# Performance work log

Measured on AMD Instinct MI355X. Metric: run time of the kernel, lower is better.

## Reference

```python
import jax, jax.numpy as jnp
import numpy as np

T, B, IN, H, A = 512, 256, 292, 128, 12


def setup_inputs() -> dict:
    key = jax.random.key(0)
    ks = jax.random.split(key, 8)
    s = 1.0 / np.sqrt(H)
    return {
        "x": jax.random.normal(ks[0], (T, B, IN), dtype=jnp.float32),
        "done": jax.random.randint(ks[1], (T, B), 0, 2, dtype=jnp.int32),
        "h0": jax.random.normal(ks[2], (1, B, H), dtype=jnp.float32),
        "c0": jax.random.normal(ks[3], (1, B, H), dtype=jnp.float32),
        "W_ih": jax.random.normal(ks[4], (4 * H, IN), dtype=jnp.float32) * s,
        "W_hh": jax.random.normal(ks[5], (4 * H, H), dtype=jnp.float32) * s,
        "b_ih": jnp.zeros((4 * H,), dtype=jnp.float32),
        "b_hh": jnp.zeros((4 * H,), dtype=jnp.float32),
        "W_pi": jax.random.normal(ks[6], (A, H), dtype=jnp.float32) * 0.01,
        "b_pi": jnp.zeros((A,), dtype=jnp.float32),
        "W_v": jax.random.normal(ks[7], (1, H), dtype=jnp.float32),
        "b_v": jnp.zeros((1,), dtype=jnp.float32),
    }


def reference(x, done, h0, c0, W_ih, W_hh, b_ih, b_hh, W_pi, b_pi, W_v, b_v):
    # get_states: per-timestep LSTM with done-based reset of (h, c), as a scan.
    done_f = done.astype(x.dtype)  # [T, B]
    bias = b_ih + b_hh  # [4H]

    def step(carry, inp):
        h, c = carry  # [B, H] each
        x_t, d_t = inp  # [B, IN], [B]
        m = (1.0 - d_t)[:, None]  # reset mask
        h = h * m
        c = c * m
        # PyTorch LSTM gate order: input, forget, cell(g), output
        gates = x_t @ W_ih.T + h @ W_hh.T + bias  # [B, 4H]
        i, f, g, o = jnp.split(gates, 4, axis=-1)
        c = jax.nn.sigmoid(f) * c + jax.nn.sigmoid(i) * jnp.tanh(g)
        h = jax.nn.sigmoid(o) * jnp.tanh(c)
        return (h, c), h

    (hN, cN), hs = jax.lax.scan(step, (h0[0], c0[0]), (x, done_f))
    hidden = hs.reshape(T * B, H)  # flatten(cat(new_hidden), 0, 1)
    logits = hidden @ W_pi.T + b_pi  # policy_layers
    value = hidden @ W_v.T + b_v  # value_layers
    return jnp.concatenate([logits, value], axis=-1)  # [T*B, A+1]
```

## Files before the change

kernel.cpp:

```cpp
#include <hip/hip_runtime.h>
#include <stdint.h>
#include <stddef.h>

#define T_ 512
#define B_ 256
#define IN_ 292
#define H_ 128
#define G4_ 512
#define TB_ 131072
#define LCH 32
#define NCH 16
#define KP_ 320

typedef short bf16x8 __attribute__((ext_vector_type(8)));
typedef float f32x4 __attribute__((ext_vector_type(4)));

__device__ __forceinline__ unsigned short f2bf(float f) {
  unsigned u = __float_as_uint(f);
  u += 0x7FFFu + ((u >> 16) & 1u);
  return (unsigned short)(u >> 16);
}
__device__ __forceinline__ float bf2f(unsigned short s) {
  return __uint_as_float(((unsigned)s) << 16);
}
__device__ __forceinline__ unsigned bfpack2(float a, float b) {
  unsigned ua = __float_as_uint(a) + 0x8000u;
  unsigned ub = __float_as_uint(b) + 0x8000u;
  return __builtin_amdgcn_perm(ub, ua, 0x07060302u);
}
__device__ __forceinline__ float sigf(float x) {
  return __builtin_amdgcn_rcpf(1.0f + __expf(-x));
}
__device__ __forceinline__ float tanhf_(float x) {
  return 1.0f - 2.0f * __builtin_amdgcn_rcpf(__expf(2.0f * x) + 1.0f);
}
__device__ __forceinline__ void barrier_lds() {
  asm volatile("s_waitcnt lgkmcnt(0)\n\ts_barrier" ::: "memory");
}
__device__ __forceinline__ void load_pr(const unsigned short* p, ushort4* pr) {
  union { uint4 v; ushort4 s[2]; } a, b;
  a.v = *(const uint4*)p;
  b.v = *(const uint4*)(p + 8);
  pr[0] = a.s[0]; pr[1] = a.s[1]; pr[2] = b.s[0]; pr[3] = b.s[1];
}

__global__ __launch_bounds__(256) void k0w_cvt(
    const float* __restrict__ Wih, const float* __restrict__ bih,
    const float* __restrict__ bhh, unsigned short* __restrict__ Wb,
    float* __restrict__ bias2) {
  const int g = blockIdx.x * 256 + threadIdx.x;
  const int jj = g / 40, s = g % 40;
  const int src = (jj & 3) * 128 + (jj >> 2);
  if (g < 512) {
    const int sb = (g & 3) * 128 + (g >> 2);
    bias2[g] = bih[sb] + bhh[sb];
  }
  float4 a = {0.f, 0.f, 0.f, 0.f}, b = {0.f, 0.f, 0.f, 0.f};
  const float* p = Wih + (size_t)src * IN_ + 8 * s;
  if (s < 36) { a = *(const float4*)p; b = *(const float4*)(p + 4); }
  else if (s == 36) { a = *(const float4*)p; }
  uint4 o;
  o.x = bfpack2(a.x, a.y); o.y = bfpack2(a.z, a.w);
  o.z = bfpack2(b.x, b.y); o.w = bfpack2(b.z, b.w);
  *(uint4*)&Wb[(size_t)jj * KP_ + 8 * s] = o;
}

__global__ __launch_bounds__(512, 2) void k1_pregemm(
    const float* __restrict__ x, const unsigned short* __restrict__ Wb,
    const float* __restrict__ bias2, unsigned short* __restrict__ pre2) {
  __shared__ unsigned short xt[2][128 * 32];

  const int m0 = blockIdx.x * 128;
  const int tid = threadIdx.x;
  const int w = tid >> 6;
  const int lane = tid & 63;
  const int l15 = lane & 15;
  const int q = lane >> 4;

  const int xrow = w * 16 + (lane >> 2);
  const int xcol = (lane & 3) * 8;
  const float* xbase = x + (size_t)(m0 + xrow) * IN_;

  f32x4 acc[4][8];
#pragma unroll
  for (int s = 0; s < 4; s++)
#pragma unroll
    for (int ms = 0; ms < 8; ms++) acc[s][ms] = (f32x4){0.f, 0.f, 0.f, 0.f};

  float4 xst[3][2];
#pragma unroll
  for (int t = 0; t < 3; t++) {
    xst[t][0] = *(const float4*)(xbase + 32 * t + xcol);
    xst[t][1] = *(const float4*)(xbase + 32 * t + xcol + 4);
  }
  bf16x8 af[4];
#pragma unroll
  for (int s = 0; s < 4; s++)
    af[s] = *(const bf16x8*)&Wb[(size_t)(w * 64 + 16 * s + l15) * KP_ + q * 8];

  {
    uint4 v;
    v.x = bfpack2(xst[0][0].x, xst[0][0].y); v.y = bfpack2(xst[0][0].z, xst[0][0].w);
    v.z = bfpack2(xst[0][1].x, xst[0][1].y); v.w = bfpack2(xst[0][1].z, xst[0][1].w);
    *(uint4*)&xt[0][xrow * 32 + xcol] = v;
  }
  barrier_lds();

#pragma unroll
  for (int it = 0; it < 10; it++) {
    bf16x8 afn[4];
    if (it < 9) {
      const int kk = 32 * (it + 1);
#pragma unroll
      for (int s = 0; s < 4; s++)
        afn[s] = *(const bf16x8*)&Wb[(size_t)(w * 64 + 16 * s + l15) * KP_ + kk + q * 8];
    }
    if (it + 3 <= 9) {
      const int tt = it + 3;
      if (tt < 9) {
        xst[it % 3][0] = *(const float4*)(xbase + 32 * tt + xcol);
        xst[it % 3][1] = *(const float4*)(xbase + 32 * tt + xcol + 4);
      } else {
        float4 z = {0.f, 0.f, 0.f, 0.f};
        xst[it % 3][0] = (xcol == 0) ? *(const float4*)(xbase + 288) : z;
        xst[it % 3][1] = z;
      }
    }
    const unsigned short* xb = xt[it & 1];
    bf16x8 bfr[8];
#pragma unroll
    for (int ms = 0; ms < 8; ms++)
      bfr[ms] = *(const bf16x8*)&xb[(16 * ms + l15) * 32 + q * 8];
#pragma unroll
    for (int s = 0; s < 4; s++)
#pragma unroll
      for (int ms = 0; ms < 8; ms++)
        acc[s][ms] = __builtin_amdgcn_mfma_f32_16x16x32_bf16(
            af[s], bfr[ms], acc[s][ms], 0, 0, 0);
    if (it < 9) {
      const float4* xs = xst[(it + 1) % 3];
      uint4 v;
      v.x = bfpack2(xs[0].x, xs[0].y); v.y = bfpack2(xs[0].z, xs[0].w);
      v.z = bfpack2(xs[1].x, xs[1].y); v.w = bfpack2(xs[1].z, xs[1].w);
      *(uint4*)&xt[(it + 1) & 1][xrow * 32 + xcol] = v;
    }
#pragma unroll
    for (int s = 0; s < 4; s++) af[s] = afn[s];
    barrier_lds();
  }

#pragma unroll
  for (int s = 0; s < 4; s++) {
    const int jjb = w * 64 + 16 * s + 4 * q;
    const float4 bb = *(const float4*)&bias2[jjb];
#pragma unroll
    for (int ms = 0; ms < 8; ms++) {
      const int m = m0 + 16 * ms + l15;
      uint2 st;
      st.x = bfpack2(acc[s][ms][0] + bb.x, acc[s][ms][1] + bb.y);
      st.y = bfpack2(acc[s][ms][2] + bb.z, acc[s][ms][3] + bb.w);
      *(uint2*)&pre2[((size_t)m << 9) + jjb] = st;
    }
  }
}

__global__ __launch_bounds__(512) void k2a_chunk(
    const unsigned short* __restrict__ pre2, const float* __restrict__ Whh,
    const int* __restrict__ done, unsigned short* __restrict__ hidden,
    unsigned short* __restrict__ hfin, float* __restrict__ cfin) {
  __shared__ unsigned short hs[2][16 * 136];
  __shared__ int dns[LCH * 16];

  const int bg = blockIdx.x & 15;
  const int ck = blockIdx.x >> 4;
  const int t0 = ck * LCH;
  const int tid = threadIdx.x;
  const int w = tid >> 6;
  const int lane = tid & 63;
  const int l15 = lane & 15;
  const int q = lane >> 4;
  const int bglob = bg * 16 + l15;
  const int kcell = 16 * w + 4 * q;
  const int kq16 = kcell * 4;

  {
    const int r = tid >> 4, c = tid & 15;
    dns[tid] = done[(size_t)(t0 + r) * B_ + bg * 16 + c];
  }

  bf16x8 wf[4][4];
#pragma unroll
  for (int tI = 0; tI < 4; tI++) {
    const int jg = 16 * (w + 8 * tI) + l15;
#pragma unroll
    for (int kc = 0; kc < 4; kc++) {
      const float* p = Whh + (size_t)jg * H_ + kc * 32 + q * 8;
      float4 u0 = *(const float4*)p;
      float4 u1 = *(const float4*)(p + 4);
      bf16x8 r;
      r[0]=(short)f2bf(u0.x); r[1]=(short)f2bf(u0.y); r[2]=(short)f2bf(u0.z); r[3]=(short)f2bf(u0.w);
      r[4]=(short)f2bf(u1.x); r[5]=(short)f2bf(u1.y); r[6]=(short)f2bf(u1.z); r[7]=(short)f2bf(u1.w);
      wf[tI][kc] = r;
    }
  }

  float c_[4] = {0.f, 0.f, 0.f, 0.f};
  {
    const int b = tid >> 5, k = (tid & 31) * 4;
    *(ushort4*)&hs[0][b * 136 + k] = (ushort4){0, 0, 0, 0};
  }
  bool vld = false;
  __syncthreads();

  ushort4 pr[4], prn[4];
  load_pr(pre2 + ((size_t)t0 * B_ + bglob) * G4_ + kq16, pr);
  load_pr(pre2 + ((size_t)(t0 + 1) * B_ + bglob) * G4_ + kq16, prn);

  ushort4 hw = {0, 0, 0, 0};
#pragma unroll 1
  for (int u = 0; u < LCH; u++) {
    const int t = t0 + u;
    ushort4 pr2[4];
    const int un = (u + 2 < LCH) ? u + 2 : LCH - 1;
    load_pr(pre2 + ((size_t)(t0 + un) * B_ + bglob) * G4_ + kq16, pr2);

    const int dn = dns[u * 16 + l15];
    vld = vld || (dn != 0);

    const unsigned short* hb = hs[u & 1];
    bf16x8 hf[4];
#pragma unroll
    for (int kc = 0; kc < 4; kc++) {
      bf16x8 v = *(const bf16x8*)&hb[l15 * 136 + kc * 32 + q * 8];
      if (dn) v = (bf16x8){0, 0, 0, 0, 0, 0, 0, 0};
      hf[kc] = v;
    }

    f32x4 acc[4];
#pragma unroll
    for (int tI = 0; tI < 4; tI++) acc[tI] = (f32x4){0.f, 0.f, 0.f, 0.f};
#pragma unroll
    for (int tI = 0; tI < 4; tI++)
#pragma unroll
      for (int kc = 0; kc < 4; kc++)
        acc[tI] = __builtin_amdgcn_mfma_f32_16x16x32_bf16(
            wf[tI][kc], hf[kc], acc[tI], 0, 0, 0);

    const float m = dn ? 0.0f : 1.0f;
    float hv[4];
#pragma unroll
    for (int r = 0; r < 4; r++) {
      const float iv = acc[0][r] + bf2f(pr[r].x);
      const float fv = acc[1][r] + bf2f(pr[r].y);
      const float gv = acc[2][r] + bf2f(pr[r].z);
      const float ov = acc[3][r] + bf2f(pr[r].w);
      float cc = c_[r] * m;
      cc = sigf(fv) * cc + sigf(iv) * tanhf_(gv);
      c_[r] = cc;
      hv[r] = sigf(ov) * tanhf_(cc);
    }
    uint2 hp = {bfpack2(hv[0], hv[1]), bfpack2(hv[2], hv[3])};
    hw = *(ushort4*)&hp;
    *(uint2*)&hs[(u + 1) & 1][l15 * 136 + kcell] = hp;
    if (vld)
      *(uint2*)&hidden[((size_t)t * B_ + bglob) * H_ + kcell] = hp;
#pragma unroll
    for (int tI = 0; tI < 4; tI++) { pr[tI] = prn[tI]; prn[tI] = pr2[tI]; }
    barrier_lds();
  }

  *(ushort4*)&hfin[((size_t)ck * B_ + bglob) * H_ + kcell] = hw;
  float4 cv = {c_[0], c_[1], c_[2], c_[3]};
  *(float4*)&cfin[((size_t)ck * B_ + bglob) * H_ + kcell] = cv;
}

__global__ __launch_bounds__(512) void k2b_par(
    const unsigned short* __restrict__ pre2, const float* __restrict__ Whh,
    const float* __restrict__ h0, const float* __restrict__ c0,
    const int* __restrict__ done, unsigned short* __restrict__ hidden,
    const unsigned short* __restrict__ hfin, const float* __restrict__ cfin,
    int* __restrict__ needfix) {
  __shared__ unsigned short hs[2][16 * 136];
  __shared__ int dns[LCH * 16];

  const int bg = blockIdx.x & 15;
  const int ck = blockIdx.x >> 4;
  const int t0 = ck * LCH;
  const int tid = threadIdx.x;
  const int w = tid >> 6;
  const int lane = tid & 63;
  const int l15 = lane & 15;
  const int q = lane >> 4;
  const int bglob = bg * 16 + l15;
  const int kcell = 16 * w + 4 * q;
  const int kq16 = kcell * 4;

  {
    const int r = tid >> 4, c = tid & 15;
    dns[tid] = done[(size_t)(t0 + r) * B_ + bg * 16 + c];
  }

  bf16x8 wf[4][4];
#pragma unroll
  for (int tI = 0; tI < 4; tI++) {
    const int jg = 16 * (w + 8 * tI) + l15;
#pragma unroll
    for (int kc = 0; kc < 4; kc++) {
      const float* p = Whh + (size_t)jg * H_ + kc * 32 + q * 8;
      float4 u0 = *(const float4*)p;
      float4 u1 = *(const float4*)(p + 4);
      bf16x8 r;
      r[0]=(short)f2bf(u0.x); r[1]=(short)f2bf(u0.y); r[2]=(short)f2bf(u0.z); r[3]=(short)f2bf(u0.w);
      r[4]=(short)f2bf(u1.x); r[5]=(short)f2bf(u1.y); r[6]=(short)f2bf(u1.z); r[7]=(short)f2bf(u1.w);
      wf[tI][kc] = r;
    }
  }

  float c_[4];
  {
    const int b = tid >> 5, k = (tid & 31) * 4;
    if (ck == 0) {
      float4 hv = *(const float4*)(h0 + (size_t)(bg * 16 + b) * H_ + k);
      uint2 hp = {bfpack2(hv.x, hv.y), bfpack2(hv.z, hv.w)};
      *(uint2*)&hs[0][b * 136 + k] = hp;
      float4 cv = *(const float4*)(c0 + (size_t)bglob * H_ + kcell);
      c_[0] = cv.x; c_[1] = cv.y; c_[2] = cv.z; c_[3] = cv.w;
    } else {
      ushort4 hv = *(const ushort4*)&hfin[((size_t)(ck - 1) * B_ + bg * 16 + b) * H_ + k];
      *(ushort4*)&hs[0][b * 136 + k] = hv;
      float4 cv = *(const float4*)&cfin[((size_t)(ck - 1) * B_ + bglob) * H_ + kcell];
      c_[0] = cv.x; c_[1] = cv.y; c_[2] = cv.z; c_[3] = cv.w;
    }
  }
  int cur = 0;
  bool act = true;
  __syncthreads();

  ushort4 pr[4];
  load_pr(pre2 + ((size_t)t0 * B_ + bglob) * G4_ + kq16, pr);

#pragma unroll 1
  for (int u = 0; u < LCH; u++) {
    const int t = t0 + u;
    const int dn = dns[u * 16 + l15];
    const bool nact = act && (dn == 0);
    if (__ballot(nact) == 0ULL) { act = false; break; }
    act = nact;

    ushort4 prn[4];
    const int un = (u + 1 < LCH) ? u + 1 : LCH - 1;
    load_pr(pre2 + ((size_t)(t0 + un) * B_ + bglob) * G4_ + kq16, prn);

    const unsigned short* hb = hs[cur];
    bf16x8 hf[4];
#pragma unroll
    for (int kc = 0; kc < 4; kc++)
      hf[kc] = *(const bf16x8*)&hb[l15 * 136 + kc * 32 + q * 8];

    f32x4 acc[4];
#pragma unroll
    for (int tI = 0; tI < 4; tI++) acc[tI] = (f32x4){0.f, 0.f, 0.f, 0.f};
#pragma unroll
    for (int tI = 0; tI < 4; tI++)
#pragma unroll
      for (int kc = 0; kc < 4; kc++)
        acc[tI] = __builtin_amdgcn_mfma_f32_16x16x32_bf16(
            wf[tI][kc], hf[kc], acc[tI], 0, 0, 0);

    float hv[4];
#pragma unroll
    for (int r = 0; r < 4; r++) {
      const float iv = acc[0][r] + bf2f(pr[r].x);
      const float fv = acc[1][r] + bf2f(pr[r].y);
      const float gv = acc[2][r] + bf2f(pr[r].z);
      const float ov = acc[3][r] + bf2f(pr[r].w);
      float cc = sigf(fv) * c_[r] + sigf(iv) * tanhf_(gv);
      c_[r] = cc;
      hv[r] = sigf(ov) * tanhf_(cc);
    }
    uint2 hp = {bfpack2(hv[0], hv[1]), bfpack2(hv[2], hv[3])};
    *(uint2*)&hs[cur ^ 1][l15 * 136 + kcell] = hp;
    if (act)
      *(uint2*)&hidden[((size_t)t * B_ + bglob) * H_ + kcell] = hp;
#pragma unroll
    for (int tI = 0; tI < 4; tI++) pr[tI] = prn[tI];
    barrier_lds();
    cur ^= 1;
  }

  if (tid == 0) needfix[blockIdx.x] = (__ballot(act) != 0ULL) ? 1 : 0;
}

__global__ __launch_bounds__(512) void k2c_guard(
    const unsigned short* __restrict__ pre2, const float* __restrict__ Whh,
    const float* __restrict__ h0, const float* __restrict__ c0,
    const int* __restrict__ done, unsigned short* __restrict__ hidden,
    const unsigned short* __restrict__ hfin, const float* __restrict__ cfin,
    const int* __restrict__ needfix) {
  const int bg = blockIdx.x;
  bool dirty = false;
  for (int c2 = 0; c2 < NCH - 1; c2++) dirty |= (needfix[c2 * 16 + bg] != 0);
  if (!dirty) return;

  __shared__ unsigned short hs[2][16 * 136];
  __shared__ int dns[T_ * 16];

  const int tid = threadIdx.x;
  const int w = tid >> 6;
  const int lane = tid & 63;
  const int l15 = lane & 15;
  const int q = lane >> 4;
  const int bglob = bg * 16 + l15;
  const int kcell = 16 * w + 4 * q;
  const int kq16 = kcell * 4;

  {
    const int* p = done + (size_t)tid * B_ + bg * 16;
    *(int4*)&dns[tid * 16]      = *(const int4*)(p);
    *(int4*)&dns[tid * 16 + 4]  = *(const int4*)(p + 4);
    *(int4*)&dns[tid * 16 + 8]  = *(const int4*)(p + 8);
    *(int4*)&dns[tid * 16 + 12] = *(const int4*)(p + 12);
  }

  bf16x8 wf[4][4];
#pragma unroll
  for (int tI = 0; tI < 4; tI++) {
    const int jg = 16 * (w + 8 * tI) + l15;
#pragma unroll
    for (int kc = 0; kc < 4; kc++) {
      const float* p = Whh + (size_t)jg * H_ + kc * 32 + q * 8;
      float4 u0 = *(const float4*)p;
      float4 u1 = *(const float4*)(p + 4);
      bf16x8 r;
      r[0]=(short)f2bf(u0.x); r[1]=(short)f2bf(u0.y); r[2]=(short)f2bf(u0.z); r[3]=(short)f2bf(u0.w);
      r[4]=(short)f2bf(u1.x); r[5]=(short)f2bf(u1.y); r[6]=(short)f2bf(u1.z); r[7]=(short)f2bf(u1.w);
      wf[tI][kc] = r;
    }
  }

  float c_[4];
  {
    float4 cv = *(const float4*)(c0 + (size_t)bglob * H_ + kcell);
    c_[0] = cv.x; c_[1] = cv.y; c_[2] = cv.z; c_[3] = cv.w;
    const int b = tid >> 5, k = (tid & 31) * 4;
    float4 hv = *(const float4*)(h0 + (size_t)(bg * 16 + b) * H_ + k);
    uint2 hp = {bfpack2(hv.x, hv.y), bfpack2(hv.z, hv.w)};
    *(uint2*)&hs[0][b * 136 + k] = hp;
  }
  int cur = 0;
  __syncthreads();

#pragma unroll 1
  for (int ck = 0; ck < NCH; ck++) {
    const int t0 = ck * LCH;
    bool act = true;

    ushort4 pr[4];
    load_pr(pre2 + ((size_t)t0 * B_ + bglob) * G4_ + kq16, pr);

#pragma unroll 1
    for (int u = 0; u < LCH; u++) {
      const int t = t0 + u;
      const int dn = dns[t * 16 + l15];
      const bool nact = act && (dn == 0);
      if (__ballot(nact) == 0ULL) { act = false; break; }
      act = nact;

      ushort4 prn[4];
      const int un = (u + 1 < LCH) ? u + 1 : LCH - 1;
      load_pr(pre2 + ((size_t)(t0 + un) * B_ + bglob) * G4_ + kq16, prn);

      const unsigned short* hb = hs[cur];
      bf16x8 hf[4];
#pragma unroll
      for (int kc = 0; kc < 4; kc++)
        hf[kc] = *(const bf16x8*)&hb[l15 * 136 + kc * 32 + q * 8];

      f32x4 acc[4];
#pragma unroll
      for (int tI = 0; tI < 4; tI++) acc[tI] = (f32x4){0.f, 0.f, 0.f, 0.f};
#pragma unroll
      for (int tI = 0; tI < 4; tI++)
#pragma unroll
        for (int kc = 0; kc < 4; kc++)
          acc[tI] = __builtin_amdgcn_mfma_f32_16x16x32_bf16(
              wf[tI][kc], hf[kc], acc[tI], 0, 0, 0);

      float hv[4];
#pragma unroll
      for (int r = 0; r < 4; r++) {
        const float iv = acc[0][r] + bf2f(pr[r].x);
        const float fv = acc[1][r] + bf2f(pr[r].y);
        const float gv = acc[2][r] + bf2f(pr[r].z);
        const float ov = acc[3][r] + bf2f(pr[r].w);
        float cc = sigf(fv) * c_[r] + sigf(iv) * tanhf_(gv);
        c_[r] = cc;
        hv[r] = sigf(ov) * tanhf_(cc);
      }
      uint2 hp = {bfpack2(hv[0], hv[1]), bfpack2(hv[2], hv[3])};
      *(uint2*)&hs[cur ^ 1][l15 * 136 + kcell] = hp;
      if (act)
        *(uint2*)&hidden[((size_t)t * B_ + bglob) * H_ + kcell] = hp;
#pragma unroll
      for (int tI = 0; tI < 4; tI++) pr[tI] = prn[tI];
      barrier_lds();
      cur ^= 1;
    }

    if (!act) {
      ushort4 hv = *(const ushort4*)&hfin[((size_t)ck * B_ + bglob) * H_ + kcell];
      float4 cv = *(const float4*)&cfin[((size_t)ck * B_ + bglob) * H_ + kcell];
      c_[0] = cv.x; c_[1] = cv.y; c_[2] = cv.z; c_[3] = cv.w;
      *(ushort4*)&hs[cur][l15 * 136 + kcell] = hv;
    }
    barrier_lds();
  }
}

__global__ __launch_bounds__(256) void k3_head(
    const unsigned short* __restrict__ hidden, const float* __restrict__ Wpi,
    const float* __restrict__ bpi, const float* __restrict__ Wv,
    const float* __restrict__ bv, float* __restrict__ out) {
  __shared__ unsigned short hs3[64 * 136];
  __shared__ float bias_s[16];

  const int tid = threadIdx.x;
  const int w = tid >> 6;
  const int lane = tid & 63;
  const int l15 = lane & 15;
  const int q = lane >> 4;
  const int m0 = blockIdx.x * 64;

  if (tid < 16) bias_s[tid] = (tid < 12) ? bpi[tid] : ((tid == 12) ? bv[0] : 0.f);

  bf16x8 wf3[4];
#pragma unroll
  for (int kc = 0; kc < 4; kc++) {
    float4 u0 = {0.f, 0.f, 0.f, 0.f}, u1 = {0.f, 0.f, 0.f, 0.f};
    if (l15 < 12) {
      const float* p = Wpi + (size_t)l15 * H_ + kc * 32 + q * 8;
      u0 = *(const float4*)p; u1 = *(const float4*)(p + 4);
    } else if (l15 == 12) {
      const float* p = Wv + kc * 32 + q * 8;
      u0 = *(const float4*)p; u1 = *(const float4*)(p + 4);
    }
    bf16x8 r;
    r[0]=(short)f2bf(u0.x); r[1]=(short)f2bf(u0.y); r[2]=(short)f2bf(u0.z); r[3]=(short)f2bf(u0.w);
    r[4]=(short)f2bf(u1.x); r[5]=(short)f2bf(u1.y); r[6]=(short)f2bf(u1.z); r[7]=(short)f2bf(u1.w);
    wf3[kc] = r;
  }

  {
    const int row = tid >> 2, ks = (tid & 3) * 32;
    const unsigned short* p = hidden + (size_t)(m0 + row) * H_ + ks;
#pragma unroll
    for (int i = 0; i < 4; i++)
      *(uint4*)&hs3[row * 136 + ks + i * 8] = *(const uint4*)(p + i * 8);
  }
  __syncthreads();

  f32x4 acc = (f32x4){0.f, 0.f, 0.f, 0.f};
#pragma unroll
  for (int kc = 0; kc < 4; kc++) {
    bf16x8 hf = *(bf16x8*)&hs3[(16 * w + l15) * 136 + kc * 32 + q * 8];
    acc = __builtin_amdgcn_mfma_f32_16x16x32_bf16(wf3[kc], hf, acc, 0, 0, 0);
  }

  const float4 bb = *(float4*)&bias_s[4 * q];
  const int m = m0 + 16 * w + l15;
  const size_t ro = (size_t)m * 13;
  float v0 = acc[0] + bb.x, v1 = acc[1] + bb.y, v2 = acc[2] + bb.z, v3 = acc[3] + bb.w;
  if (q < 3) {
    out[ro + 4 * q + 0] = v0;
    out[ro + 4 * q + 1] = v1;
    out[ro + 4 * q + 2] = v2;
    out[ro + 4 * q + 3] = v3;
  } else {
    out[ro + 12] = v0;
  }
}

extern "C" void kernel_launch(void* const* d_in, const int* in_sizes, int n_in,
                              void* d_out, int out_size, void* d_ws, size_t ws_size,
                              hipStream_t stream) {
  const float* x    = (const float*)d_in[0];
  const int* done   = (const int*)d_in[1];
  const float* h0   = (const float*)d_in[2];
  const float* c0   = (const float*)d_in[3];
  const float* Wih  = (const float*)d_in[4];
  const float* Whh  = (const float*)d_in[5];
  const float* bih  = (const float*)d_in[6];
  const float* bhh  = (const float*)d_in[7];
  const float* Wpi  = (const float*)d_in[8];
  const float* bpi  = (const float*)d_in[9];
  const float* Wv   = (const float*)d_in[10];
  const float* bv   = (const float*)d_in[11];
  (void)in_sizes; (void)n_in; (void)out_size; (void)ws_size;

  unsigned short* pre2 = (unsigned short*)d_ws;
  unsigned short* hidden = pre2 + (size_t)TB_ * G4_;
  unsigned short* Wb   = (unsigned short*)d_out;
  float* bias2         = (float*)((char*)d_out + (512u << 10));
  unsigned short* hfin = (unsigned short*)((char*)d_out + (1u << 20));
  float* cfin          = (float*)((char*)d_out + (2u << 20));
  int* needfix         = (int*)((char*)d_out + (4u << 20));
  float* out = (float*)d_out;

  k0w_cvt<<<80, 256, 0, stream>>>(Wih, bih, bhh, Wb, bias2);
  k1_pregemm<<<TB_ / 128, 512, 0, stream>>>(x, Wb, bias2, pre2);
  k2a_chunk<<<256, 512, 0, stream>>>(pre2, Whh, done, hidden, hfin, cfin);
  k2b_par<<<256, 512, 0, stream>>>(pre2, Whh, h0, c0, done, hidden, hfin, cfin, needfix);
  k2c_guard<<<16, 512, 0, stream>>>(pre2, Whh, h0, c0, done, hidden, hfin, cfin, needfix);
  k3_head<<<TB_ / 64, 256, 0, stream>>>(hidden, Wpi, bpi, Wv, bv, out);
}
```

Measured before the change: 430.9 us.

## Split pre-GEMM across 16 waves and stage epilogue through LDS for coalesced stores

The input-projection GEMM kernel moves from 8 waves (each a 64x128 output tile) to 16 waves in a 2x8 grid, each holding a 64x64 tile. This halves accumulator registers per wave and should raise occupancy. The weight-fragment register prefetch is dropped in favour of loading per iteration, and the x prefetch depth goes from three stages to two. The epilogue now writes bf16 results into an LDS staging buffer and stores full 1 KB rows to global memory with coalesced 16-byte writes. This adds 16 extra barriers and a larger shared-memory footprint.

Measured after the change: 423.1 us. About the same (-1.8%).

```diff
diff --git a/kernel.cpp b/kernel.cpp
--- a/kernel.cpp
+++ b/kernel.cpp
@@ -65,102 +65,103 @@
   *(uint4*)&Wb[(size_t)jj * KP_ + 8 * s] = o;
 }
 
-__global__ __launch_bounds__(512, 2) void k1_pregemm(
+__global__ __launch_bounds__(1024, 4) void k1_pregemm(
     const float* __restrict__ x, const unsigned short* __restrict__ Wb,
     const float* __restrict__ bias2, unsigned short* __restrict__ pre2) {
   __shared__ unsigned short xt[2][128 * 32];
+  __shared__ unsigned short ep[16 * 520];
 
   const int m0 = blockIdx.x * 128;
   const int tid = threadIdx.x;
   const int w = tid >> 6;
+  const int wr = w >> 3;
+  const int wc = w & 7;
   const int lane = tid & 63;
   const int l15 = lane & 15;
   const int q = lane >> 4;
 
-  const int xrow = w * 16 + (lane >> 2);
-  const int xcol = (lane & 3) * 8;
+  const int xrow = tid >> 3;
+  const int xcol = (tid & 7) * 4;
   const float* xbase = x + (size_t)(m0 + xrow) * IN_;
 
-  f32x4 acc[4][8];
+  f32x4 acc[4][4];
 #pragma unroll
   for (int s = 0; s < 4; s++)
 #pragma unroll
-    for (int ms = 0; ms < 8; ms++) acc[s][ms] = (f32x4){0.f, 0.f, 0.f, 0.f};
-
-  float4 xst[3][2];
-#pragma unroll
-  for (int t = 0; t < 3; t++) {
-    xst[t][0] = *(const float4*)(xbase + 32 * t + xcol);
-    xst[t][1] = *(const float4*)(xbase + 32 * t + xcol + 4);
-  }
-  bf16x8 af[4];
-#pragma unroll
-  for (int s = 0; s < 4; s++)
-    af[s] = *(const bf16x8*)&Wb[(size_t)(w * 64 + 16 * s + l15) * KP_ + q * 8];
-
-  {
-    uint4 v;
-    v.x = bfpack2(xst[0][0].x, xst[0][0].y); v.y = bfpack2(xst[0][0].z, xst[0][0].w);
-    v.z = bfpack2(xst[0][1].x, xst[0][1].y); v.w = bfpack2(xst[0][1].z, xst[0][1].w);
-    *(uint4*)&xt[0][xrow * 32 + xcol] = v;
+    for (int ms = 0; ms < 4; ms++) acc[s][ms] = (f32x4){0.f, 0.f, 0.f, 0.f};
+
+  float4 xst[2];
+  xst[0] = *(const float4*)(xbase + xcol);
+  xst[1] = *(const float4*)(xbase + 32 + xcol);
+  {
+    uint2 v;
+    v.x = bfpack2(xst[0].x, xst[0].y);
+    v.y = bfpack2(xst[0].z, xst[0].w);
+    *(uint2*)&xt[0][xrow * 32 + xcol] = v;
   }
   barrier_lds();
 
 #pragma unroll
   for (int it = 0; it < 10; it++) {
-    bf16x8 afn[4];
-    if (it < 9) {
-      const int kk = 32 * (it + 1);
-#pragma unroll
-      for (int s = 0; s < 4; s++)
-        afn[s] = *(const bf16x8*)&Wb[(size_t)(w * 64 + 16 * s + l15) * KP_ + kk + q * 8];
-    }
-    if (it + 3 <= 9) {
-      const int tt = it + 3;
+    if (it + 2 <= 9) {
+      const int tt = it + 2;
       if (tt < 9) {
-        xst[it % 3][0] = *(const float4*)(xbase + 32 * tt + xcol);
-        xst[it % 3][1] = *(const float4*)(xbase + 32 * tt + xcol + 4);
+        xst[it & 1] = *(const float4*)(xbase + 32 * tt + xcol);
       } else {
         float4 z = {0.f, 0.f, 0.f, 0.f};
-        xst[it % 3][0] = (xcol == 0) ? *(const float4*)(xbase + 288) : z;
-        xst[it % 3][1] = z;
+        xst[it & 1] = (xcol == 0) ? *(const float4*)(xbase + 288) : z;
       }
     }
+    bf16x8 af[4];
+    const int kk = 32 * it;
+#pragma unroll
+    for (int s = 0; s < 4; s++)
+      af[s] = *(const bf16x8*)&Wb[(size_t)(wc * 64 + 16 * s + l15) * KP_ + kk + q * 8];
     const unsigned short* xb = xt[it & 1];
-    bf16x8 bfr[8];
-#pragma unroll
-    for (int ms = 0; ms < 8; ms++)
-      bfr[ms] = *(const bf16x8*)&xb[(16 * ms + l15) * 32 + q * 8];
+    bf16x8 bfr[4];
+#pragma unroll
+    for (int ms = 0; ms < 4; ms++)
+      bfr[ms] = *(const bf16x8*)&xb[(64 * wr + 16 * ms + l15) * 32 + q * 8];
 #pragma unroll
     for (int s = 0; s < 4; s++)
 #pragma unroll
-      for (int ms = 0; ms < 8; ms++)
+      for (int ms = 0; ms < 4; ms++)
         acc[s][ms] = __builtin_amdgcn_mfma_f32_16x16x32_bf16(
             af[s], bfr[ms], acc[s][ms], 0, 0, 0);
     if (it < 9) {
-      const float4* xs = xst[(it + 1) % 3];
-      uint4 v;
-      v.x = bfpack2(xs[0].x, xs[0].y); v.y = bfpack2(xs[0].z, xs[0].w);
-      v.z = bfpack2(xs[1].x, xs[1].y); v.w = bfpack2(xs[1].z, xs[1].w);
-      *(uint4*)&xt[(it + 1) & 1][xrow * 32 + xcol] = v;
-    }
-#pragma unroll
-    for (int s = 0; s < 4; s++) af[s] = afn[s];
+      const float4 xv = xst[(it + 1) & 1];
+      uint2 v;
+      v.x = bfpack2(xv.x, xv.y);
+      v.y = bfpack2(xv.z, xv.w);
+      *(uint2*)&xt[(it + 1) & 1][xrow * 32 + xcol] = v;
+    }
     barrier_lds();
   }
 
-#pragma unroll
-  for (int s = 0; s < 4; s++) {
-    const int jjb = w * 64 + 16 * s + 4 * q;
-    const float4 bb = *(const float4*)&bias2[jjb];
-#pragma unroll
-    for (int ms = 0; ms < 8; ms++) {
-      const int m = m0 + 16 * ms + l15;
-      uint2 st;
-      st.x = bfpack2(acc[s][ms][0] + bb.x, acc[s][ms][1] + bb.y);
-      st.y = bfpack2(acc[s][ms][2] + bb.z, acc[s][ms][3] + bb.w);
-      *(uint2*)&pre2[((size_t)m << 9) + jjb] = st;
-    }
+  float4 bb[4];
+#pragma unroll
+  for (int s = 0; s < 4; s++)
+    bb[s] = *(const float4*)&bias2[wc * 64 + 16 * s + 4 * q];
+
+#pragma unroll
+  for (int st = 0; st < 8; st++) {
+    if ((st >> 2) == wr) {
+      const int ms = st & 3;
+#pragma unroll
+      for (int s = 0; s < 4; s++) {
+        uint2 v;
+        v.x = bfpack2(acc[s][ms][0] + bb[s].x, acc[s][ms][1] + bb[s].y);
+        v.y = bfpack2(acc[s][ms][2] + bb[s].z, acc[s][ms][3] + bb[s].w);
+        *(uint2*)&ep[l15 * 520 + wc * 64 + s * 16 + q * 4] = v;
+      }
+    }
+    barrier_lds();
+    {
+      const int off = lane;
+      uint4 v = *(const uint4*)&ep[w * 520 + off * 8];
+      *(uint4*)&pre2[((size_t)(m0 + 16 * st + w) << 9) + off * 8] = v;
+    }
+    barrier_lds();
   }
 }
 
@@ -607,7 +608,7 @@
   float* out = (float*)d_out;
 
   k0w_cvt<<<80, 256, 0, stream>>>(Wih, bih, bhh, Wb, bias2);
-  k1_pregemm<<<TB_ / 128, 512, 0, stream>>>(x, Wb, bias2, pre2);
+  k1_pregemm<<<TB_ / 128, 1024, 0, stream>>>(x, Wb, bias2, pre2);
   k2a_chunk<<<256, 512, 0, stream>>>(pre2, Whh, done, hidden, hfin, cfin);
   k2b_par<<<256, 512, 0, stream>>>(pre2, Whh, h0, c0, done, hidden, hfin, cfin, needfix);
   k2c_guard<<<16, 512, 0, stream>>>(pre2, Whh, h0, c0, done, hidden, hfin, cfin, needfix);
```

## Persist pregemm blocks over four M-tiles with fragment-ordered weights and LDS-staged stores

Applied to the files above, without the earlier changes.

The weight conversion kernel now writes W_ih in MFMA-fragment order, so each lane's A-operand load is contiguous. The input-projection GEMM is relaunched with 256 blocks, each looping over four 128-row tiles with a continuous x prefetch pipeline. The x LDS tile is padded to a 40-element stride to reduce bank conflicts. Each tile's output is staged through a large LDS buffer so pre2 is written in full 1 KB rows rather than scattered 8-byte stores. The extra ~66 KB of LDS and the non-unrolled loop may reduce occupancy, and the grid is smaller, in exchange for coalesced writes and amortized startup.

After: 400.4 us. 1.08x faster.

```diff
diff --git a/kernel.cpp b/kernel.cpp
--- a/kernel.cpp
+++ b/kernel.cpp
@@ -46,40 +46,62 @@
 
 __global__ __launch_bounds__(256) void k0w_cvt(
     const float* __restrict__ Wih, const float* __restrict__ bih,
-    const float* __restrict__ bhh, unsigned short* __restrict__ Wb,
+    const float* __restrict__ bhh, unsigned short* __restrict__ Wf,
     float* __restrict__ bias2) {
   const int g = blockIdx.x * 256 + threadIdx.x;
-  const int jj = g / 40, s = g % 40;
+  const int lane = g & 63;
+  const int rest = g >> 6;
+  const int it = rest % 10;
+  const int g16 = rest / 10;
+  const int jj = g16 * 16 + (lane & 15);
   const int src = (jj & 3) * 128 + (jj >> 2);
+  const int c0 = it * 32 + (lane >> 4) * 8;
   if (g < 512) {
     const int sb = (g & 3) * 128 + (g >> 2);
     bias2[g] = bih[sb] + bhh[sb];
   }
   float4 a = {0.f, 0.f, 0.f, 0.f}, b = {0.f, 0.f, 0.f, 0.f};
-  const float* p = Wih + (size_t)src * IN_ + 8 * s;
-  if (s < 36) { a = *(const float4*)p; b = *(const float4*)(p + 4); }
-  else if (s == 36) { a = *(const float4*)p; }
+  const float* p = Wih + (size_t)src * IN_ + c0;
+  if (c0 + 8 <= IN_) { a = *(const float4*)p; b = *(const float4*)(p + 4); }
+  else if (c0 < IN_) { a = *(const float4*)p; }
   uint4 o;
   o.x = bfpack2(a.x, a.y); o.y = bfpack2(a.z, a.w);
   o.z = bfpack2(b.x, b.y); o.w = bfpack2(b.z, b.w);
-  *(uint4*)&Wb[(size_t)jj * KP_ + 8 * s] = o;
+  *(uint4*)&Wf[(size_t)g * 8] = o;
+}
+
+__device__ __forceinline__ void k1_xissue(
+    const float* __restrict__ x, int bid4, int xrow, int xcq, int g2,
+    float4* xa, float4* xbv) {
+  const int jx = g2 / 10, itx = g2 % 10;
+  const float* p = x + (size_t)((bid4 + jx) * 128 + xrow) * IN_ + itx * 32 + xcq;
+  const float4 z = {0.f, 0.f, 0.f, 0.f};
+  if (itx < 9) {
+    xa[g2 & 1] = *(const float4*)p;
+    xbv[g2 & 1] = *(const float4*)(p + 4);
+  } else {
+    xa[g2 & 1] = (xcq == 0) ? *(const float4*)p : z;
+    xbv[g2 & 1] = z;
+  }
 }
 
 __global__ __launch_bounds__(512, 2) void k1_pregemm(
-    const float* __restrict__ x, const unsigned short* __restrict__ Wb,
+    const float* __restrict__ x, const unsigned short* __restrict__ Wf,
     const float* __restrict__ bias2, unsigned short* __restrict__ pre2) {
-  __shared__ unsigned short xt[2][128 * 32];
-
-  const int m0 = blockIdx.x * 128;
+  __shared__ unsigned short xt[2][128 * 40];
+  __shared__ unsigned short ep[64 * 520];
+
   const int tid = threadIdx.x;
   const int w = tid >> 6;
   const int lane = tid & 63;
   const int l15 = lane & 15;
   const int q = lane >> 4;
-
-  const int xrow = w * 16 + (lane >> 2);
-  const int xcol = (lane & 3) * 8;
-  const float* xbase = x + (size_t)(m0 + xrow) * IN_;
+  const int bid4 = blockIdx.x * 4;
+
+  const int xrow = tid >> 2;
+  const int xcq = (tid & 3) * 8;
+
+  const unsigned short* wfbase = Wf + ((size_t)(4 * w) * 10 * 64 + lane) * 8;
 
   f32x4 acc[4][8];
 #pragma unroll
@@ -87,79 +109,88 @@
 #pragma unroll
     for (int ms = 0; ms < 8; ms++) acc[s][ms] = (f32x4){0.f, 0.f, 0.f, 0.f};
 
-  float4 xst[3][2];
-#pragma unroll
-  for (int t = 0; t < 3; t++) {
-    xst[t][0] = *(const float4*)(xbase + 32 * t + xcol);
-    xst[t][1] = *(const float4*)(xbase + 32 * t + xcol + 4);
-  }
+  float4 xa[2], xbv[2];
+  k1_xissue(x, bid4, xrow, xcq, 0, xa, xbv);
+  k1_xissue(x, bid4, xrow, xcq, 1, xa, xbv);
   bf16x8 af[4];
 #pragma unroll
   for (int s = 0; s < 4; s++)
-    af[s] = *(const bf16x8*)&Wb[(size_t)(w * 64 + 16 * s + l15) * KP_ + q * 8];
-
+    af[s] = *(const bf16x8*)(wfbase + (s * 10 + 0) * 512);
   {
     uint4 v;
-    v.x = bfpack2(xst[0][0].x, xst[0][0].y); v.y = bfpack2(xst[0][0].z, xst[0][0].w);
-    v.z = bfpack2(xst[0][1].x, xst[0][1].y); v.w = bfpack2(xst[0][1].z, xst[0][1].w);
-    *(uint4*)&xt[0][xrow * 32 + xcol] = v;
+    v.x = bfpack2(xa[0].x, xa[0].y); v.y = bfpack2(xa[0].z, xa[0].w);
+    v.z = bfpack2(xbv[0].x, xbv[0].y); v.w = bfpack2(xbv[0].z, xbv[0].w);
+    *(uint4*)&xt[0][xrow * 40 + xcq] = v;
   }
   barrier_lds();
 
-#pragma unroll
-  for (int it = 0; it < 10; it++) {
+#pragma unroll 1
+  for (int git = 0; git < 40; ++git) {
+    const int it = git % 10;
     bf16x8 afn[4];
-    if (it < 9) {
-      const int kk = 32 * (it + 1);
+    if (git < 39) {
+      const int nit = (it == 9) ? 0 : it + 1;
 #pragma unroll
       for (int s = 0; s < 4; s++)
-        afn[s] = *(const bf16x8*)&Wb[(size_t)(w * 64 + 16 * s + l15) * KP_ + kk + q * 8];
-    }
-    if (it + 3 <= 9) {
-      const int tt = it + 3;
-      if (tt < 9) {
-        xst[it % 3][0] = *(const float4*)(xbase + 32 * tt + xcol);
-        xst[it % 3][1] = *(const float4*)(xbase + 32 * tt + xcol + 4);
-      } else {
-        float4 z = {0.f, 0.f, 0.f, 0.f};
-        xst[it % 3][0] = (xcol == 0) ? *(const float4*)(xbase + 288) : z;
-        xst[it % 3][1] = z;
-      }
-    }
-    const unsigned short* xb = xt[it & 1];
+        afn[s] = *(const bf16x8*)(wfbase + (s * 10 + nit) * 512);
+    }
+    if (git + 2 < 40) k1_xissue(x, bid4, xrow, xcq, git + 2, xa, xbv);
+    const unsigned short* xb = xt[git & 1];
     bf16x8 bfr[8];
 #pragma unroll
     for (int ms = 0; ms < 8; ms++)
-      bfr[ms] = *(const bf16x8*)&xb[(16 * ms + l15) * 32 + q * 8];
+      bfr[ms] = *(const bf16x8*)&xb[(16 * ms + l15) * 40 + q * 8];
 #pragma unroll
     for (int s = 0; s < 4; s++)
 #pragma unroll
       for (int ms = 0; ms < 8; ms++)
         acc[s][ms] = __builtin_amdgcn_mfma_f32_16x16x32_bf16(
             af[s], bfr[ms], acc[s][ms], 0, 0, 0);
-    if (it < 9) {
-      const float4* xs = xst[(it + 1) % 3];
+    if (git < 39) {
+      const float4 A = xa[(git + 1) & 1], Bv = xbv[(git + 1) & 1];
       uint4 v;
-      v.x = bfpack2(xs[0].x, xs[0].y); v.y = bfpack2(xs[0].z, xs[0].w);
-      v.z = bfpack2(xs[1].x, xs[1].y); v.w = bfpack2(xs[1].z, xs[1].w);
-      *(uint4*)&xt[(it + 1) & 1][xrow * 32 + xcol] = v;
+      v.x = bfpack2(A.x, A.y); v.y = bfpack2(A.z, A.w);
+      v.z = bfpack2(Bv.x, Bv.y); v.w = bfpack2(Bv.z, Bv.w);
+      *(uint4*)&xt[(git + 1) & 1][xrow * 40 + xcq] = v;
     }
 #pragma unroll
     for (int s = 0; s < 4; s++) af[s] = afn[s];
     barrier_lds();
-  }
-
-#pragma unroll
-  for (int s = 0; s < 4; s++) {
-    const int jjb = w * 64 + 16 * s + 4 * q;
-    const float4 bb = *(const float4*)&bias2[jjb];
-#pragma unroll
-    for (int ms = 0; ms < 8; ms++) {
-      const int m = m0 + 16 * ms + l15;
-      uint2 st;
-      st.x = bfpack2(acc[s][ms][0] + bb.x, acc[s][ms][1] + bb.y);
-      st.y = bfpack2(acc[s][ms][2] + bb.z, acc[s][ms][3] + bb.w);
-      *(uint2*)&pre2[((size_t)m << 9) + jjb] = st;
+
+    if (it == 9) {
+      const int m0 = (bid4 + git / 10) * 128;
+      float4 bb[4];
+#pragma unroll
+      for (int s = 0; s < 4; s++)
+        bb[s] = *(const float4*)&bias2[64 * w + 16 * s + 4 * q];
+#pragma unroll
+      for (int st = 0; st < 2; ++st) {
+#pragma unroll
+        for (int mm = 0; mm < 4; ++mm) {
+          const int ms = 4 * st + mm;
+#pragma unroll
+          for (int s = 0; s < 4; ++s) {
+            uint2 v;
+            v.x = bfpack2(acc[s][ms][0] + bb[s].x, acc[s][ms][1] + bb[s].y);
+            v.y = bfpack2(acc[s][ms][2] + bb[s].z, acc[s][ms][3] + bb[s].w);
+            *(uint2*)&ep[(16 * mm + l15) * 520 + 64 * w + 16 * s + 4 * q] = v;
+          }
+        }
+        barrier_lds();
+#pragma unroll
+        for (int p = 0; p < 8; ++p) {
+          const int r = 8 * p + w;
+          uint4 v = *(const uint4*)&ep[r * 520 + lane * 8];
+          *(uint4*)&pre2[((size_t)(m0 + 64 * st + r) << 9) + lane * 8] = v;
+        }
+        barrier_lds();
+      }
+      if (git < 39) {
+#pragma unroll
+        for (int s = 0; s < 4; s++)
+#pragma unroll
+          for (int ms = 0; ms < 8; ms++) acc[s][ms] = (f32x4){0.f, 0.f, 0.f, 0.f};
+      }
     }
   }
 }
@@ -599,15 +630,15 @@
 
   unsigned short* pre2 = (unsigned short*)d_ws;
   unsigned short* hidden = pre2 + (size_t)TB_ * G4_;
-  unsigned short* Wb   = (unsigned short*)d_out;
+  unsigned short* Wf   = (unsigned short*)d_out;
   float* bias2         = (float*)((char*)d_out + (512u << 10));
   unsigned short* hfin = (unsigned short*)((char*)d_out + (1u << 20));
   float* cfin          = (float*)((char*)d_out + (2u << 20));
   int* needfix         = (int*)((char*)d_out + (4u << 20));
   float* out = (float*)d_out;
 
-  k0w_cvt<<<80, 256, 0, stream>>>(Wih, bih, bhh, Wb, bias2);
-  k1_pregemm<<<TB_ / 128, 512, 0, stream>>>(x, Wb, bias2, pre2);
+  k0w_cvt<<<80, 256, 0, stream>>>(Wih, bih, bhh, Wf, bias2);
+  k1_pregemm<<<256, 512, 0, stream>>>(x, Wf, bias2, pre2);
   k2a_chunk<<<256, 512, 0, stream>>>(pre2, Whh, done, hidden, hfin, cfin);
   k2b_par<<<256, 512, 0, stream>>>(pre2, Whh, h0, c0, done, hidden, hfin, cfin, needfix);
   k2c_guard<<<16, 512, 0, stream>>>(pre2, Whh, h0, c0, done, hidden, hfin, cfin, needfix);
```
